# Performance work log

Hardware: AMD Instinct MI355X
Metric: run time of the kernel (lower is better)

## Reference

```python
import jax, jax.numpy as jnp
import numpy as np

# 4x4 Walsh-Hadamard matrix in natural (Hadamard/Kronecker) order: H4 = H2 (x) H2
_H4 = jnp.array([[1, 1, 1, 1],
                 [1, -1, 1, -1],
                 [1, 1, -1, -1],
                 [1, -1, -1, 1]], dtype=jnp.float32)

T = 16          # number of 2D WHT coefficients (4x4 block)
BLK = 4         # spatial block size


def _iwht_stream(trans, weight):
    """trans: (16, B, nH, nW, C); weight: (16, C, K) -> out: (B, 4*nH, 4*nW, K).

    Per-coefficient channel mixing in the transform domain, then inverse 2D
    Walsh-Hadamard transform (separable, scale 1/16) back to spatial domain.
    """
    _, B, nH, nW, C = trans.shape
    K = weight.shape[2]
    # transform-domain channel mixing: (t,b,h,w,c) x (t,c,k) -> (t,b,h,w,k)
    mixed = jnp.einsum('tbhwc,tck->tbhwk', trans, weight)
    # split coefficient index t = 4*u + v (row/col frequency)
    mixed = mixed.reshape(BLK, BLK, B, nH, nW, K)
    # inverse separable WHT: out[b,nh,i,nw,j,k] = (1/16) sum_{u,v} H4[i,u] H4[j,v] mixed[u,v,...]
    out = jnp.einsum('iu,jv,uvbhwk->bhiwjk', _H4, _H4, mixed) * (1.0 / 16.0)
    return out.reshape(B, nH * BLK, nW * BLK, K)


def setup_inputs() -> dict:
    key = jax.random.key(0)
    k1, k2, k3, k4 = jax.random.split(key, 4)
    B, nH, nW, C = 16, 28, 28, 64
    out_channels = 128
    K1 = out_channels // 2
    K2 = out_channels // 2 + out_channels % 2
    transIm1 = jax.random.normal(k1, (T, B, nH, nW, C), dtype=jnp.float32)
    transIm2 = jax.random.normal(k2, (T, B, nH, nW, C), dtype=jnp.float32)
    weight1 = jax.random.normal(k3, (T, C, K1), dtype=jnp.float32) * 0.02
    weight2 = jax.random.normal(k4, (T, C, K2), dtype=jnp.float32) * 0.02
    bias1 = jnp.zeros((1, 1, 1, K1), dtype=jnp.float32)
    bias2 = jnp.zeros((1, 1, 1, K2), dtype=jnp.float32)
    return {"transIm1": transIm1, "transIm2": transIm2,
            "weight1": weight1, "weight2": weight2,
            "bias1": bias1, "bias2": bias2}


def reference(transIm1, transIm2, weight1, weight2, bias1, bias2):
    out1 = _iwht_stream(transIm1, weight1) + bias1
    out2 = _iwht_stream(transIm2, weight2) + bias2
    return (out1, out2)
```

## Files before the change

kernel.cpp:

```cpp
#include <hip/hip_runtime.h>

typedef float          f32x4 __attribute__((ext_vector_type(4)));
typedef short          s16x8 __attribute__((ext_vector_type(8)));
typedef unsigned short u16x4 __attribute__((ext_vector_type(4)));

#define NPIX       12544
#define OUT_STRIDE 12845056

__device__ __forceinline__ unsigned short f2bf(float x) {
    union { float f; unsigned u; } un; un.f = x;
    unsigned r = un.u + 0x7FFFu + ((un.u >> 16) & 1u);
    return (unsigned short)(r >> 16);
}

__global__ __launch_bounds__(256) void repack_weights(
        const float* __restrict__ w1, const float* __restrict__ w2,
        unsigned short* __restrict__ wf) {
    int gid = blockIdx.x * 256 + threadIdx.x;
    int e  = gid & 7;
    int l  = (gid >> 3) & 63;
    int nt = (gid >> 9) & 3;
    int ks = (gid >> 11) & 1;
    int t  = (gid >> 12) & 15;
    int s  = (gid >> 16) & 1;
    int c = ks * 32 + (l >> 4) * 8 + e;
    int k = nt * 16 + (l & 15);
    const float* __restrict__ w = s ? w2 : w1;
    wf[gid] = f2bf(w[(t * 64 + c) * 64 + k] * 0.0625f);
}

__global__ __launch_bounds__(256, 3) void iwht_main(
        const float* __restrict__ trans1, const float* __restrict__ trans2,
        const unsigned short* __restrict__ wf,
        const float* __restrict__ bias1, const float* __restrict__ bias2,
        float* __restrict__ out) {
    __shared__ char Alds[16 * 16 * 144];

    const int tid = threadIdx.x;
    const int bid = blockIdx.x;
    const int s   = blockIdx.y;

    const float* __restrict__ trans = s ? trans2 : trans1;
    const float* __restrict__ bias  = s ? bias2  : bias1;
    const int p0 = bid * 16;

    {
        const int p  = tid >> 4;
        const int cc = tid & 15;
        f32x4 v[16];
        #pragma unroll
        for (int t = 0; t < 16; ++t) {
            const f32x4* src = (const f32x4*)(trans + ((size_t)t * NPIX + p0) * 64);
            v[t] = src[tid];
        }
        #pragma unroll
        for (int t = 0; t < 16; ++t) {
            u16x4 h;
            h[0] = f2bf(v[t][0]); h[1] = f2bf(v[t][1]);
            h[2] = f2bf(v[t][2]); h[3] = f2bf(v[t][3]);
            *(u16x4*)(Alds + (t * 16 + p) * 144 + cc * 8) = h;
        }
    }
    __syncthreads();

    const int wid  = tid >> 6;
    const int lane = tid & 63;
    const int lrow = lane & 15;
    const int lhi  = lane >> 4;

    const s16x8* __restrict__ wb = (const s16x8*)wf;

    f32x4 o[4][4];
    #pragma unroll
    for (int i = 0; i < 4; ++i)
        #pragma unroll
        for (int j = 0; j < 4; ++j)
            o[i][j] = (f32x4){0.f, 0.f, 0.f, 0.f};

    #pragma unroll 1
    for (int u = 0; u < 4; ++u) {
        f32x4 g0 = {0.f,0.f,0.f,0.f}, g1 = {0.f,0.f,0.f,0.f};
        f32x4 g2 = {0.f,0.f,0.f,0.f}, g3 = {0.f,0.f,0.f,0.f};
        #pragma unroll
        for (int v = 0; v < 4; ++v) {
            const int t = u * 4 + v;
            const char* ap = Alds + (t * 16 + lrow) * 144 + lhi * 16;
            s16x8 a0 = *(const s16x8*)(ap);
            s16x8 a1 = *(const s16x8*)(ap + 64);
            const int bidx = (((s * 16 + t) * 2 + 0) * 4 + wid) * 64 + lane;
            s16x8 b0 = wb[bidx];
            s16x8 b1 = wb[bidx + 256];
            f32x4 acc = {0.f, 0.f, 0.f, 0.f};
            acc = __builtin_amdgcn_mfma_f32_16x16x32_bf16(a0, b0, acc, 0, 0, 0);
            acc = __builtin_amdgcn_mfma_f32_16x16x32_bf16(a1, b1, acc, 0, 0, 0);
            g0 += acc;
            if (v == 0) { g1 += acc; g2 += acc; g3 += acc; }
            if (v == 1) { g1 -= acc; g2 += acc; g3 -= acc; }
            if (v == 2) { g1 += acc; g2 -= acc; g3 -= acc; }
            if (v == 3) { g1 -= acc; g2 -= acc; g3 += acc; }
        }
        const float s1 = (u & 1) ? -1.f : 1.f;
        const float s2 = (u & 2) ? -1.f : 1.f;
        const float s3 = s1 * s2;
        #pragma unroll
        for (int j = 0; j < 4; ++j) {
            f32x4 gj = (j == 0) ? g0 : ((j == 1) ? g1 : ((j == 2) ? g2 : g3));
            o[0][j] += gj;
            o[1][j] += s1 * gj;
            o[2][j] += s2 * gj;
            o[3][j] += s3 * gj;
        }
    }

    const int k  = wid * 16 + lrow;
    const float bk = bias[k];
    const int bimg = bid / 49;
    const int hw0  = (bid % 49) * 16;
    float* __restrict__ outp = out + (s ? (size_t)OUT_STRIDE : 0);

    size_t rbase[4];
    #pragma unroll
    for (int r = 0; r < 4; ++r) {
        int hw = hw0 + lhi * 4 + r;
        int h = hw / 28, w = hw % 28;
        rbase[r] = ((size_t)(bimg * 112 + h * 4) * 112 + (w * 4)) * 64 + k;
    }
    #pragma unroll
    for (int i = 0; i < 4; ++i)
        #pragma unroll
        for (int j = 0; j < 4; ++j) {
            #pragma unroll
            for (int r = 0; r < 4; ++r)
                outp[rbase[r] + (size_t)((i * 112 + j) * 64)] = o[i][j][r] + bk;
        }
}

extern "C" void kernel_launch(void* const* d_in, const int* in_sizes, int n_in,
                              void* d_out, int out_size, void* d_ws, size_t ws_size,
                              hipStream_t stream) {
    const float* t1 = (const float*)d_in[0];
    const float* t2 = (const float*)d_in[1];
    const float* w1 = (const float*)d_in[2];
    const float* w2 = (const float*)d_in[3];
    const float* b1 = (const float*)d_in[4];
    const float* b2 = (const float*)d_in[5];
    unsigned short* wfrag = (unsigned short*)d_ws;
    float* out = (float*)d_out;

    repack_weights<<<dim3(512), dim3(256), 0, stream>>>(w1, w2, wfrag);
    iwht_main<<<dim3(784, 2), dim3(256), 0, stream>>>(t1, t2, wfrag, b1, b2, out);
}
```

Baseline: 204.4 us.

## Load activations directly into MFMA registers, dropping the LDS staging and barrier

The main kernel no longer stages the bf16-converted activation tile through shared memory. Each lane loads its fp32 A-fragment straight from global memory per u-group and converts it in registers with the HIP bf16 intrinsic. This removes the LDS writes and reads and the block barrier, and the occupancy hint rises from 3 to 4. The weight repack is rewritten to read coalesced and scatter its writes. The cost is less regular global loads per lane (two 32-byte chunks per coefficient) and more register pressure from the staged fp32 values.

```diff
diff --git a/kernel.cpp b/kernel.cpp
--- a/kernel.cpp
+++ b/kernel.cpp
@@ -1,10 +1,11 @@
 #include <hip/hip_runtime.h>
+#include <hip/hip_bf16.h>
 
-typedef float          f32x4 __attribute__((ext_vector_type(4)));
-typedef short          s16x8 __attribute__((ext_vector_type(8)));
-typedef unsigned short u16x4 __attribute__((ext_vector_type(4)));
+typedef float f32x4 __attribute__((ext_vector_type(4)));
+typedef short s16x8 __attribute__((ext_vector_type(8)));
 
 #define NPIX       12544
+#define TPLANE     802816
 #define OUT_STRIDE 12845056
 
 __device__ __forceinline__ unsigned short f2bf(float x) {
@@ -13,62 +14,50 @@
     return (unsigned short)(r >> 16);
 }
 
+__device__ __forceinline__ short bfs(float x) {
+    __hip_bfloat16 h = __float2bfloat16(x);
+    return *reinterpret_cast<short*>(&h);
+}
+
 __global__ __launch_bounds__(256) void repack_weights(
         const float* __restrict__ w1, const float* __restrict__ w2,
         unsigned short* __restrict__ wf) {
     int gid = blockIdx.x * 256 + threadIdx.x;
-    int e  = gid & 7;
-    int l  = (gid >> 3) & 63;
-    int nt = (gid >> 9) & 3;
-    int ks = (gid >> 11) & 1;
-    int t  = (gid >> 12) & 15;
-    int s  = (gid >> 16) & 1;
-    int c = ks * 32 + (l >> 4) * 8 + e;
-    int k = nt * 16 + (l & 15);
+    int k = gid & 63;
+    int c = (gid >> 6) & 63;
+    int t = (gid >> 12) & 15;
+    int s = (gid >> 16) & 1;
     const float* __restrict__ w = s ? w2 : w1;
-    wf[gid] = f2bf(w[(t * 64 + c) * 64 + k] * 0.0625f);
+    float val = w[gid & 65535] * 0.0625f;
+    int e = c & 7, lhi = (c >> 3) & 3, ks = c >> 5;
+    int l  = lhi * 16 + (k & 15);
+    int nt = k >> 4;
+    int dst = ((((s * 16 + t) * 2 + ks) * 4 + nt) * 64 + l) * 8 + e;
+    wf[dst] = f2bf(val);
 }
 
-__global__ __launch_bounds__(256, 3) void iwht_main(
+__global__ __launch_bounds__(256, 4) void iwht_main(
         const float* __restrict__ trans1, const float* __restrict__ trans2,
         const unsigned short* __restrict__ wf,
         const float* __restrict__ bias1, const float* __restrict__ bias2,
         float* __restrict__ out) {
-    __shared__ char Alds[16 * 16 * 144];
-
     const int tid = threadIdx.x;
     const int bid = blockIdx.x;
     const int s   = blockIdx.y;
-
-    const float* __restrict__ trans = s ? trans2 : trans1;
-    const float* __restrict__ bias  = s ? bias2  : bias1;
-    const int p0 = bid * 16;
-
-    {
-        const int p  = tid >> 4;
-        const int cc = tid & 15;
-        f32x4 v[16];
-        #pragma unroll
-        for (int t = 0; t < 16; ++t) {
-            const f32x4* src = (const f32x4*)(trans + ((size_t)t * NPIX + p0) * 64);
-            v[t] = src[tid];
-        }
-        #pragma unroll
-        for (int t = 0; t < 16; ++t) {
-            u16x4 h;
-            h[0] = f2bf(v[t][0]); h[1] = f2bf(v[t][1]);
-            h[2] = f2bf(v[t][2]); h[3] = f2bf(v[t][3]);
-            *(u16x4*)(Alds + (t * 16 + p) * 144 + cc * 8) = h;
-        }
-    }
-    __syncthreads();
 
     const int wid  = tid >> 6;
     const int lane = tid & 63;
     const int lrow = lane & 15;
     const int lhi  = lane >> 4;
 
-    const s16x8* __restrict__ wb = (const s16x8*)wf;
+    const float* __restrict__ trans = s ? trans2 : trans1;
+    const float* __restrict__ bias  = s ? bias2  : bias1;
+
+    const f32x4* __restrict__ abase =
+        (const f32x4*)(trans + ((size_t)(bid * 16 + lrow)) * 64 + lhi * 8);
+
+    const s16x8* __restrict__ wb =
+        (const s16x8*)wf + (size_t)s * 8192 + wid * 64 + lane;
 
     f32x4 o[4][4];
     #pragma unroll
@@ -79,17 +68,31 @@
 
     #pragma unroll 1
     for (int u = 0; u < 4; ++u) {
+        f32x4 st[4][4];
+        #pragma unroll
+        for (int v = 0; v < 4; ++v) {
+            const int t = u * 4 + v;
+            const f32x4* ap = abase + (size_t)t * (TPLANE / 4);
+            st[v][0] = ap[0];
+            st[v][1] = ap[1];
+            st[v][2] = ap[8];
+            st[v][3] = ap[9];
+        }
         f32x4 g0 = {0.f,0.f,0.f,0.f}, g1 = {0.f,0.f,0.f,0.f};
         f32x4 g2 = {0.f,0.f,0.f,0.f}, g3 = {0.f,0.f,0.f,0.f};
         #pragma unroll
         for (int v = 0; v < 4; ++v) {
             const int t = u * 4 + v;
-            const char* ap = Alds + (t * 16 + lrow) * 144 + lhi * 16;
-            s16x8 a0 = *(const s16x8*)(ap);
-            s16x8 a1 = *(const s16x8*)(ap + 64);
-            const int bidx = (((s * 16 + t) * 2 + 0) * 4 + wid) * 64 + lane;
-            s16x8 b0 = wb[bidx];
-            s16x8 b1 = wb[bidx + 256];
+            s16x8 a0, a1;
+            #pragma unroll
+            for (int e = 0; e < 4; ++e) {
+                a0[e]     = bfs(st[v][0][e]);
+                a0[e + 4] = bfs(st[v][1][e]);
+                a1[e]     = bfs(st[v][2][e]);
+                a1[e + 4] = bfs(st[v][3][e]);
+            }
+            s16x8 b0 = wb[t * 512];
+            s16x8 b1 = wb[t * 512 + 256];
             f32x4 acc = {0.f, 0.f, 0.f, 0.f};
             acc = __builtin_amdgcn_mfma_f32_16x16x32_bf16(a0, b0, acc, 0, 0, 0);
             acc = __builtin_amdgcn_mfma_f32_16x16x32_bf16(a1, b1, acc, 0, 0, 0);
```

New measurement: 243.5 us. +19.1%, slower.
